# Kernel tuning notes

Measured on AMD Instinct MI355X. Metric: run time of the kernel, lower is better.

The kernel has to match this reference:

```python
import jax, jax.numpy as jnp
import numpy as np

H = 8          # num_heads
DM = 128       # dmodel
BN_EPS = 1e-5


def _linear(x, w, b):
    # w stored as [in, out]
    return x @ w + b


def _relu_mha(q, k, v, qw, qb, kw, kb, vw, vb, ow, ob, mask):
    """TemMulHeadAtte: ReLU on projected Q/K/V, masked softmax, ReLU out-proj.
    q,k: [B,N,T,2*DM]; v: [B,N,T,DM]; mask: broadcastable to [B,N,H,T,T] or None."""
    B, N, T, _ = q.shape
    Q = jax.nn.relu(_linear(q, qw, qb)).reshape(B, N, T, H, -1)  # e = 2*DM/H
    K = jax.nn.relu(_linear(k, kw, kb)).reshape(B, N, T, H, -1)
    V = jax.nn.relu(_linear(v, vw, vb)).reshape(B, N, T, H, -1)  # d = DM/H
    scale = 1.0 / np.sqrt(Q.shape[-1]).astype(np.float32)
    scores = jnp.einsum('bnthe,bnshe->bnhts', Q, K)
    if mask is not None:
        scores = jnp.where(mask, -jnp.inf, scores)
    attn = jax.nn.softmax(scale * scores, axis=-1)  # dropout p=0 -> identity
    out = jnp.einsum('bnhts,bnshd->bnthd', attn, V).reshape(B, N, T, -1)
    return jax.nn.relu(_linear(out, ow, ob))


def setup_inputs() -> dict:
    key = jax.random.key(0)
    ks = iter(jax.random.split(key, 32))
    B, N, T = 16, 207, 24
    def w(shape, scale=0.05):
        return (jax.random.normal(next(ks), shape, dtype=jnp.float32) * scale)
    inp = {
        'x': w((B, N, T, DM), 1.0),
        'hidden': w((B, N, T, DM), 1.0),
        'tXin': w((B, N, T, DM), 1.0),
    }
    dk = 2 * DM // H * H   # 256
    dv = DM // H * H       # 128
    for pre in ('s', 't'):  # space / temporal attention params
        inp[pre + 'q_w'] = w((2 * DM, dk)); inp[pre + 'q_b'] = w((dk,))
        inp[pre + 'k_w'] = w((2 * DM, dk)); inp[pre + 'k_b'] = w((dk,))
        inp[pre + 'v_w'] = w((DM, dv));     inp[pre + 'v_b'] = w((dv,))
        inp[pre + 'o_w'] = w((dv, DM));     inp[pre + 'o_b'] = w((DM,))
    inp['gate_w'] = w((2 * DM, DM)); inp['gate_b'] = w((DM,))
    inp['bn_gamma'] = jnp.ones((DM,), jnp.float32)
    inp['bn_beta'] = jnp.zeros((DM,), jnp.float32)
    return inp


def reference(x, hidden, tXin,
              sq_w, sq_b, sk_w, sk_b, sv_w, sv_b, so_w, so_b,
              tq_w, tq_b, tk_w, tk_b, tv_w, tv_b, to_w, to_b,
              gate_w, gate_b, bn_gamma, bn_beta):
    B, N, T, E = hidden.shape
    ht = jnp.concatenate([hidden, tXin], axis=3)  # [B,N,T,2*DM]
    # spatial attention: attend over nodes (N<->T permute)
    sqk = ht.transpose(0, 2, 1, 3)        # [B,T,N,2*DM]
    sval = hidden.transpose(0, 2, 1, 3)   # [B,T,N,DM]
    spaceOut = _relu_mha(sqk, sqk, sval, sq_w, sq_b, sk_w, sk_b, sv_w, sv_b,
                         so_w, so_b, None).transpose(0, 2, 1, 3)  # [B,N,T,DM]
    # temporal attention with causal (strict upper-tri) mask
    mask = jnp.triu(jnp.ones((T, T), dtype=bool), 1)[None, None, None]
    tempOut = _relu_mha(ht, ht, hidden, tq_w, tq_b, tk_w, tk_b, tv_w, tv_b,
                        to_w, to_b, mask)  # [B,N,T,DM]
    # gate + BatchNorm2d over channel dim (training-mode batch stats, biased var)
    gi = _linear(jnp.concatenate([spaceOut, tempOut], axis=3), gate_w, gate_b)
    mean = gi.mean(axis=(0, 1, 2))
    var = gi.var(axis=(0, 1, 2))
    z = jax.nn.sigmoid((gi - mean) * jax.lax.rsqrt(var + BN_EPS) * bn_gamma + bn_beta)
    return z * spaceOut + (1.0 - z) * tempOut
```

## Files before the change

kernel.cpp:

```cpp
#include <hip/hip_runtime.h>
#include <hip/hip_bf16.h>

typedef __bf16 bf16;
typedef __bf16 bf16x8 __attribute__((ext_vector_type(8)));
typedef float f32x4 __attribute__((ext_vector_type(4)));

#define MTOT 79488
#define NDIM 207
#define TDIM 24

__global__ void detect_dtype(const void* __restrict__ hidden, int* __restrict__ flag)
{
    __shared__ int cnt;
    if (threadIdx.x == 0) cnt = 0;
    __syncthreads();
    const bf16* h = (const bf16*)hidden;
    int local = 0;
    for (int i = threadIdx.x; i < 4096; i += 256) {
        float v = (float)h[i];
        if (!(fabsf(v) < 1e6f)) local++;
    }
    atomicAdd(&cnt, local);
    __syncthreads();
    if (threadIdx.x == 0) *flag = (cnt > 8) ? 1 : 0;
}

__device__ inline float ld_ext(const void* p, int idx, int isF32)
{
    return isF32 ? ((const float*)p)[idx] : (float)((const bf16*)p)[idx];
}

__global__ __launch_bounds__(256) void prep_weights(
    const void* __restrict__ sq, const void* __restrict__ sk, const void* __restrict__ sv,
    const void* __restrict__ so, const void* __restrict__ tq, const void* __restrict__ tk,
    const void* __restrict__ tv, const void* __restrict__ to_, const void* __restrict__ gw,
    const void* __restrict__ sqb, const void* __restrict__ skb, const void* __restrict__ svb,
    const void* __restrict__ sob, const void* __restrict__ tqb, const void* __restrict__ tkb,
    const void* __restrict__ tvb, const void* __restrict__ tob, const void* __restrict__ gb,
    bf16* __restrict__ wdst, bf16* __restrict__ bdst, const int* __restrict__ dtf)
{
    const int isF32 = *dtf;
    if (blockIdx.x == 1536) {
        for (int j = threadIdx.x; j < 1664; j += 256) {
            const void* src; int i2;
            if      (j < 256)  { src = sqb; i2 = j; }
            else if (j < 512)  { src = skb; i2 = j - 256; }
            else if (j < 640)  { src = svb; i2 = j - 512; }
            else if (j < 896)  { src = tqb; i2 = j - 640; }
            else if (j < 1152) { src = tkb; i2 = j - 896; }
            else if (j < 1280) { src = tvb; i2 = j - 1152; }
            else if (j < 1408) { src = sob; i2 = j - 1280; }
            else if (j < 1536) { src = tob; i2 = j - 1408; }
            else               { src = gb;  i2 = j - 1536; }
            bdst[j] = (bf16)ld_ext(src, i2, isF32);
        }
        return;
    }
    const int e = blockIdx.x * 256 + threadIdx.x;
    float v;
    if (e < 327680) {
        int br = (e >= 163840);
        int e2 = e - br * 163840;
        int n = e2 >> 8, k = e2 & 255;
        const void* qw = br ? tq : sq;
        const void* kw = br ? tk : sk;
        const void* vw = br ? tv : sv;
        if      (n < 256) v = ld_ext(qw, k * 256 + n, isF32);
        else if (n < 512) v = ld_ext(kw, k * 256 + (n - 256), isF32);
        else              v = (k < 128) ? ld_ext(vw, k * 128 + (n - 512), isF32) : 0.f;
    } else if (e < 360448) {
        int br = (e >= 344064);
        int e2 = e - 327680 - br * 16384;
        int n = e2 >> 7, k = e2 & 127;
        v = ld_ext(br ? to_ : so, k * 128 + n, isF32);
    } else {
        int e2 = e - 360448;
        int n = e2 >> 8, k = e2 & 255;
        v = ld_ext(gw, k * 128 + n, isF32);
    }
    wdst[e] = (bf16)v;
}

__global__ __launch_bounds__(256) void gemm_bt(
    const void* __restrict__ A0v, const void* __restrict__ A1v,
    const bf16* __restrict__ Bt, const bf16* __restrict__ bias,
    bf16* __restrict__ C, int Nout, int Ktot, int doRelu, int aExt,
    const int* __restrict__ dtf)
{
    const int isF32 = *dtf;
    const int aF32  = aExt & isF32;
    __shared__ bf16 As[128 * 72];
    __shared__ bf16 Bs[128 * 72];
    const int tid  = threadIdx.x;
    const int wid  = tid >> 6, lane = tid & 63;
    const int wm   = (wid >> 1) * 64, wn = (wid & 1) * 64;
    const int quad = lane >> 4, l16 = lane & 15;
    const int m0   = blockIdx.x * 128, n0 = blockIdx.y * 128;
    const int lrow = tid >> 3;
    const int lcol = (tid & 7) * 8;

    f32x4 acc[4][4] = {};

    for (int k0 = 0; k0 < Ktot; k0 += 64) {
        const void* Ap = (k0 < 128) ? A0v : A1v;
        const int koff = (k0 < 128) ? k0 : k0 - 128;
        #pragma unroll
        for (int p = 0; p < 4; ++p) {
            int r = lrow + p * 32;
            bf16x8 av;
            if (aF32) {
                const float* Af = (const float*)Ap;
                f32x4 lo = *(const f32x4*)(Af + (size_t)(m0 + r) * 128 + koff + lcol);
                f32x4 hi = *(const f32x4*)(Af + (size_t)(m0 + r) * 128 + koff + lcol + 4);
                av[0]=(bf16)lo[0]; av[1]=(bf16)lo[1]; av[2]=(bf16)lo[2]; av[3]=(bf16)lo[3];
                av[4]=(bf16)hi[0]; av[5]=(bf16)hi[1]; av[6]=(bf16)hi[2]; av[7]=(bf16)hi[3];
            } else {
                av = *(const bf16x8*)((const bf16*)Ap + (size_t)(m0 + r) * 128 + koff + lcol);
            }
            *(bf16x8*)&As[r * 72 + lcol] = av;
        }
        #pragma unroll
        for (int p = 0; p < 4; ++p) {
            int r = lrow + p * 32;
            *(bf16x8*)&Bs[r * 72 + lcol] =
                *(const bf16x8*)(Bt + (size_t)(n0 + r) * Ktot + k0 + lcol);
        }
        __syncthreads();
        #pragma unroll
        for (int kk = 0; kk < 64; kk += 32) {
            bf16x8 af[4], bfr[4];
            #pragma unroll
            for (int i = 0; i < 4; ++i)
                af[i] = *(const bf16x8*)&As[(wm + i * 16 + l16) * 72 + kk + quad * 8];
            #pragma unroll
            for (int j = 0; j < 4; ++j)
                bfr[j] = *(const bf16x8*)&Bs[(wn + j * 16 + l16) * 72 + kk + quad * 8];
            #pragma unroll
            for (int i = 0; i < 4; ++i)
                #pragma unroll
                for (int j = 0; j < 4; ++j)
                    acc[i][j] = __builtin_amdgcn_mfma_f32_16x16x32_bf16(
                        af[i], bfr[j], acc[i][j], 0, 0, 0);
        }
        __syncthreads();
    }
    #pragma unroll
    for (int j = 0; j < 4; ++j) {
        int col = n0 + wn + j * 16 + l16;
        float bv = (float)bias[col];
        #pragma unroll
        for (int i = 0; i < 4; ++i) {
            int rbase = m0 + wm + i * 16 + quad * 4;
            #pragma unroll
            for (int r = 0; r < 4; ++r) {
                float v = acc[i][j][r] + bv;
                if (doRelu) v = fmaxf(v, 0.f);
                C[(size_t)(rbase + r) * Nout + col] = (bf16)v;
            }
        }
    }
}

__global__ __launch_bounds__(256) void attn_spatial_mfma(
    const bf16* __restrict__ QKV, bf16* __restrict__ O)
{
    const int hh = blockIdx.x, t = blockIdx.y, b = blockIdx.z;
    __shared__ bf16 Ks[224 * 40];
    __shared__ bf16 Vt[16 * 232];
    __shared__ bf16 Pl[4][16 * 40];
    const int tid = threadIdx.x;
    const int wave = tid >> 6, lane = tid & 63;
    const int quad = lane >> 4, l16 = lane & 15;
    const int STR = 640;

    for (int idx = tid; idx < 224 * 4; idx += 256) {
        int n = idx >> 2, seg = (idx & 3) * 8;
        bf16x8 v8 = {};
        if (n < NDIM)
            v8 = *(const bf16x8*)(QKV + ((size_t)(b * NDIM + n) * TDIM + t) * STR
                                  + 256 + hh * 32 + seg);
        *(bf16x8*)&Ks[n * 40 + seg] = v8;
    }
    for (int idx = tid; idx < 224 * 16; idx += 256) {
        int s = idx >> 4, d = idx & 15;
        bf16 v = (bf16)0.f;
        if (s < NDIM)
            v = QKV[((size_t)(b * NDIM + s) * TDIM + t) * STR + 512 + hh * 16 + d];
        Vt[d * 232 + s] = v;
    }
    __syncthreads();

    const float scale = 0.17677669529663687f;

    for (int qt = wave; qt < 13; qt += 4) {
        const int q0 = qt * 16;
        int qrow = q0 + l16; if (qrow >= NDIM) qrow = NDIM - 1;
        bf16x8 qfrag = *(const bf16x8*)(QKV + ((size_t)(b * NDIM + qrow) * TDIM + t) * STR
                                        + hh * 32 + quad * 8);
        f32x4 s[14];
        #pragma unroll
        for (int c = 0; c < 14; ++c) {
            bf16x8 kf = *(const bf16x8*)&Ks[(c * 16 + l16) * 40 + quad * 8];
            f32x4 z = {};
            s[c] = __builtin_amdgcn_mfma_f32_16x16x32_bf16(qfrag, kf, z, 0, 0, 0);
        }
        float l[4];
        #pragma unroll
        for (int r = 0; r < 4; ++r) {
            float mx = -1e30f;
            #pragma unroll
            for (int c = 0; c < 14; ++c) {
                int si = c * 16 + l16;
                float x = (si < NDIM) ? s[c][r] : -1e30f;
                mx = fmaxf(mx, x);
            }
            mx = fmaxf(mx, __shfl_xor(mx, 1));
            mx = fmaxf(mx, __shfl_xor(mx, 2));
            mx = fmaxf(mx, __shfl_xor(mx, 4));
            mx = fmaxf(mx, __shfl_xor(mx, 8));
            float sum = 0.f;
            #pragma unroll
            for (int c = 0; c < 14; ++c) {
                int si = c * 16 + l16;
                float p = (si < NDIM) ? __expf((s[c][r] - mx) * scale) : 0.f;
                s[c][r] = p;
                sum += p;
            }
            sum += __shfl_xor(sum, 1);
            sum += __shfl_xor(sum, 2);
            sum += __shfl_xor(sum, 4);
            sum += __shfl_xor(sum, 8);
            l[r] = sum;
        }
        f32x4 oacc = {};
        #pragma unroll
        for (int sc = 0; sc < 7; ++sc) {
            #pragma unroll
            for (int r = 0; r < 4; ++r) {
                Pl[wave][(quad * 4 + r) * 40 + l16]      = (bf16)s[2 * sc][r];
                Pl[wave][(quad * 4 + r) * 40 + 16 + l16] = (bf16)s[2 * sc + 1][r];
            }
            bf16x8 pf = *(const bf16x8*)&Pl[wave][l16 * 40 + quad * 8];
            bf16x8 vf = *(const bf16x8*)&Vt[l16 * 232 + sc * 32 + quad * 8];
            oacc = __builtin_amdgcn_mfma_f32_16x16x32_bf16(pf, vf, oacc, 0, 0, 0);
        }
        #pragma unroll
        for (int r = 0; r < 4; ++r) {
            int row = q0 + quad * 4 + r;
            if (row < NDIM)
                O[((size_t)(b * NDIM + row) * TDIM + t) * 128 + hh * 16 + l16]
                    = (bf16)(oacc[r] / l[r]);
        }
    }
}

__global__ __launch_bounds__(256) void attn_temporal(
    const bf16* __restrict__ QKV, bf16* __restrict__ O)
{
    const size_t m0 = (size_t)blockIdx.x * TDIM;
    __shared__ float Ks[TDIM][256];
    __shared__ float Vs[TDIM][128];
    const int tid = threadIdx.x;
    const int STR = 640;

    for (int idx = tid; idx < TDIM * 32; idx += 256) {
        int row = idx >> 5, c8 = (idx & 31) * 8;
        bf16x8 v = *(const bf16x8*)(QKV + (m0 + row) * STR + 256 + c8);
        #pragma unroll
        for (int j = 0; j < 8; ++j) Ks[row][c8 + j] = (float)v[j];
    }
    for (int idx = tid; idx < TDIM * 16; idx += 256) {
        int row = idx >> 4, c8 = (idx & 15) * 8;
        bf16x8 v = *(const bf16x8*)(QKV + (m0 + row) * STR + 512 + c8);
        #pragma unroll
        for (int j = 0; j < 8; ++j) Vs[row][c8 + j] = (float)v[j];
    }
    __syncthreads();

    if (tid < 8 * TDIM) {
        const int h = tid / TDIM, q = tid % TDIM;
        float qv[32];
        const bf16x8* qp = (const bf16x8*)(QKV + (m0 + q) * STR + h * 32);
        #pragma unroll
        for (int cc = 0; cc < 4; ++cc) {
            bf16x8 v = qp[cc];
            #pragma unroll
            for (int jj = 0; jj < 8; ++jj) qv[cc * 8 + jj] = (float)v[jj];
        }
        const float scale = 0.17677669529663687f;
        float mx = -1e29f, l = 0.f, acc[16] = {};
        for (int s = 0; s <= q; ++s) {
            float x = 0.f;
            #pragma unroll
            for (int c = 0; c < 32; ++c) x += qv[c] * Ks[s][h * 32 + c];
            x *= scale;
            float mn = fmaxf(mx, x);
            float corr = __expf(mx - mn);
            float p = __expf(x - mn);
            l = l * corr + p;
            #pragma unroll
            for (int d = 0; d < 16; ++d) acc[d] = acc[d] * corr + p * Vs[s][h * 16 + d];
            mx = mn;
        }
        float inv = 1.f / l;
        #pragma unroll
        for (int d = 0; d < 16; ++d)
            O[(m0 + q) * 128 + h * 16 + d] = (bf16)(acc[d] * inv);
    }
}

__global__ __launch_bounds__(256) void bn_stats(
    const bf16* __restrict__ gi, float* __restrict__ stats)
{
    __shared__ float ssum[256], ssq[256];
    const size_t base = (size_t)blockIdx.x * 16384;
    const int tid = threadIdx.x;
    float s = 0.f, sq = 0.f;
    #pragma unroll 4
    for (int i = 0; i < 64; ++i) {
        float v = (float)gi[base + (size_t)i * 256 + tid];
        s += v; sq += v * v;
    }
    ssum[tid] = s; ssq[tid] = sq;
    __syncthreads();
    if (tid < 128) {
        atomicAdd(&stats[tid], ssum[tid] + ssum[tid + 128]);
        atomicAdd(&stats[128 + tid], ssq[tid] + ssq[tid + 128]);
    }
}

__global__ __launch_bounds__(256) void bn_final(
    const bf16* __restrict__ gi, const bf16* __restrict__ sp, const bf16* __restrict__ tp,
    const void* __restrict__ gammav, const void* __restrict__ betav,
    const float* __restrict__ stats, void* __restrict__ outv,
    const int* __restrict__ dtf)
{
    const int isF32 = *dtf;
    const int idx = blockIdx.x * 256 + threadIdx.x;
    const int c = idx & 127;
    const float invM = 1.f / (float)MTOT;
    float mean = stats[c] * invM;
    float var  = stats[128 + c] * invM - mean * mean;
    float gam = ld_ext(gammav, c, isF32);
    float bet = ld_ext(betav, c, isF32);
    float g = (float)gi[idx];
    float zn = (g - mean) * rsqrtf(var + 1e-5f) * gam + bet;
    float z = 1.f / (1.f + __expf(-zn));
    float s = (float)sp[idx], t = (float)tp[idx];
    float r = z * s + (1.f - z) * t;
    if (isF32) ((float*)outv)[idx] = r;
    else       ((bf16*)outv)[idx] = (bf16)r;
}

extern "C" void kernel_launch(void* const* d_in, const int* in_sizes, int n_in,
                              void* d_out, int out_size, void* d_ws, size_t ws_size,
                              hipStream_t stream)
{
    const void* hidden = d_in[1];
    const void* tXin   = d_in[2];
    const void* sq_w = d_in[3];  const void* sq_b = d_in[4];
    const void* sk_w = d_in[5];  const void* sk_b = d_in[6];
    const void* sv_w = d_in[7];  const void* sv_b = d_in[8];
    const void* so_w = d_in[9];  const void* so_b = d_in[10];
    const void* tq_w = d_in[11]; const void* tq_b = d_in[12];
    const void* tk_w = d_in[13]; const void* tk_b = d_in[14];
    const void* tv_w = d_in[15]; const void* tv_b = d_in[16];
    const void* to_w = d_in[17]; const void* to_b = d_in[18];
    const void* gate_w = d_in[19]; const void* gate_b = d_in[20];
    const void* gamma  = d_in[21]; const void* beta   = d_in[22];

    char* ws = (char*)d_ws;
    float* stats = (float*)ws;
    int*  dtf    = (int*)(ws + 1024);
    bf16* bB     = (bf16*)(ws + 2048);
    bf16* wT     = (bf16*)(ws + 8192);
    bf16* spaceO = (bf16*)(ws + 794624);
    bf16* attnO  = (bf16*)(ws + 21143552);
    bf16* QKV    = (bf16*)(ws + 41492480);
    bf16* tempO  = attnO;
    bf16* gi     = QKV;

    bf16* sW  = wT;            bf16* tW  = wT + 163840;
    bf16* soT = wT + 327680;   bf16* toT = wT + 344064;
    bf16* gwT = wT + 360448;

    hipMemsetAsync(stats, 0, 1024, stream);
    detect_dtype<<<1, 256, 0, stream>>>(hidden, dtf);
    prep_weights<<<dim3(1537), 256, 0, stream>>>(
        sq_w, sk_w, sv_w, so_w, tq_w, tk_w, tv_w, to_w, gate_w,
        sq_b, sk_b, sv_b, so_b, tq_b, tk_b, tv_b, to_b, gate_b,
        wT, bB, dtf);

    gemm_bt<<<dim3(621, 5), 256, 0, stream>>>(hidden, tXin, sW, bB, QKV, 640, 256, 1, 1, dtf);
    attn_spatial_mfma<<<dim3(8, TDIM, 16), 256, 0, stream>>>(QKV, attnO);
    gemm_bt<<<dim3(621, 1), 256, 0, stream>>>(attnO, nullptr, soT, bB + 1280, spaceO, 128, 128, 1, 0, dtf);

    gemm_bt<<<dim3(621, 5), 256, 0, stream>>>(hidden, tXin, tW, bB + 640, QKV, 640, 256, 1, 1, dtf);
    attn_temporal<<<dim3(16 * NDIM), 256, 0, stream>>>(QKV, attnO);
    gemm_bt<<<dim3(621, 1), 256, 0, stream>>>(attnO, nullptr, toT, bB + 1408, tempO, 128, 128, 1, 0, dtf);

    gemm_bt<<<dim3(621, 1), 256, 0, stream>>>(spaceO, tempO, gwT, bB + 1536, gi, 128, 256, 0, 0, dtf);
    bn_stats<<<dim3(621), 256, 0, stream>>>(gi, stats);
    bn_final<<<dim3(39744), 256, 0, stream>>>(gi, spaceO, tempO, gamma, beta, stats, d_out, dtf);
}
```

Before: 572.6 us.

## Use MFMA for temporal attention and pre-convert fp32 inputs to bf16

Replaces the scalar per-thread temporal attention loop with an MFMA-based kernel. Each wave handles two heads, computes masked scores with bf16 matrix instructions, does a shuffle-based softmax and runs a PV MFMA. Separately, when the workspace is large enough, hidden and tXin are converted once to bf16 buffers. This lets the two QKV GEMMs read bf16 A operands instead of converting fp32 on every tile load. The conversion adds an extra pass over the inputs, and the bf16 probabilities may lose precision.

```diff
diff --git a/kernel.cpp b/kernel.cpp
--- a/kernel.cpp
+++ b/kernel.cpp
@@ -28,6 +28,26 @@
 __device__ inline float ld_ext(const void* p, int idx, int isF32)
 {
     return isF32 ? ((const float*)p)[idx] : (float)((const bf16*)p)[idx];
+}
+
+__global__ __launch_bounds__(256) void cvt_inputs(
+    const void* __restrict__ hidden, const void* __restrict__ tXin,
+    bf16* __restrict__ hb, bf16* __restrict__ tb, const int* __restrict__ dtf)
+{
+    const int isF32 = *dtf;
+    const void* src = blockIdx.y ? tXin : hidden;
+    bf16* dst = blockIdx.y ? tb : hb;
+    const size_t e8 = ((size_t)blockIdx.x * 256 + threadIdx.x) * 8;
+    bf16x8 v;
+    if (isF32) {
+        f32x4 lo = *(const f32x4*)((const float*)src + e8);
+        f32x4 hi = *(const f32x4*)((const float*)src + e8 + 4);
+        v[0]=(bf16)lo[0]; v[1]=(bf16)lo[1]; v[2]=(bf16)lo[2]; v[3]=(bf16)lo[3];
+        v[4]=(bf16)hi[0]; v[5]=(bf16)hi[1]; v[6]=(bf16)hi[2]; v[7]=(bf16)hi[3];
+    } else {
+        v = *(const bf16x8*)((const bf16*)src + e8);
+    }
+    *(bf16x8*)(dst + e8) = v;
 }
 
 __global__ __launch_bounds__(256) void prep_weights(
@@ -87,8 +107,7 @@
     bf16* __restrict__ C, int Nout, int Ktot, int doRelu, int aExt,
     const int* __restrict__ dtf)
 {
-    const int isF32 = *dtf;
-    const int aF32  = aExt & isF32;
+    const int aF32 = aExt & *dtf;
     __shared__ bf16 As[128 * 72];
     __shared__ bf16 Bs[128 * 72];
     const int tid  = threadIdx.x;
@@ -254,58 +273,81 @@
     }
 }
 
-__global__ __launch_bounds__(256) void attn_temporal(
+__global__ __launch_bounds__(256) void attn_temporal_mfma(
     const bf16* __restrict__ QKV, bf16* __restrict__ O)
 {
     const size_t m0 = (size_t)blockIdx.x * TDIM;
-    __shared__ float Ks[TDIM][256];
-    __shared__ float Vs[TDIM][128];
+    __shared__ bf16 Khs[8 * 32 * 40];
+    __shared__ bf16 Vts[8 * 16 * 40];
+    __shared__ bf16 Pl[4][16 * 40];
     const int tid = threadIdx.x;
+    const int wave = tid >> 6, lane = tid & 63;
+    const int quad = lane >> 4, l16 = lane & 15;
     const int STR = 640;
 
-    for (int idx = tid; idx < TDIM * 32; idx += 256) {
-        int row = idx >> 5, c8 = (idx & 31) * 8;
-        bf16x8 v = *(const bf16x8*)(QKV + (m0 + row) * STR + 256 + c8);
-        #pragma unroll
-        for (int j = 0; j < 8; ++j) Ks[row][c8 + j] = (float)v[j];
-    }
-    for (int idx = tid; idx < TDIM * 16; idx += 256) {
-        int row = idx >> 4, c8 = (idx & 15) * 8;
-        bf16x8 v = *(const bf16x8*)(QKV + (m0 + row) * STR + 512 + c8);
-        #pragma unroll
-        for (int j = 0; j < 8; ++j) Vs[row][c8 + j] = (float)v[j];
+    for (int idx = tid; idx < 32 * 32; idx += 256) {
+        int row = idx >> 5, seg = idx & 31;
+        int h = seg >> 2, j = (seg & 3) * 8;
+        bf16x8 v8 = {};
+        if (row < TDIM)
+            v8 = *(const bf16x8*)(QKV + (m0 + row) * STR + 256 + h * 32 + j);
+        *(bf16x8*)&Khs[h * 1280 + row * 40 + j] = v8;
+    }
+    for (int idx = tid; idx < 32 * 128; idx += 256) {
+        int s = idx >> 7, c = idx & 127;
+        int h = c >> 4, d = c & 15;
+        bf16 v = (bf16)0.f;
+        if (s < TDIM) v = QKV[(m0 + s) * STR + 512 + h * 16 + d];
+        Vts[h * 640 + d * 40 + s] = v;
     }
     __syncthreads();
 
-    if (tid < 8 * TDIM) {
-        const int h = tid / TDIM, q = tid % TDIM;
-        float qv[32];
-        const bf16x8* qp = (const bf16x8*)(QKV + (m0 + q) * STR + h * 32);
-        #pragma unroll
-        for (int cc = 0; cc < 4; ++cc) {
-            bf16x8 v = qp[cc];
-            #pragma unroll
-            for (int jj = 0; jj < 8; ++jj) qv[cc * 8 + jj] = (float)v[jj];
-        }
-        const float scale = 0.17677669529663687f;
-        float mx = -1e29f, l = 0.f, acc[16] = {};
-        for (int s = 0; s <= q; ++s) {
-            float x = 0.f;
-            #pragma unroll
-            for (int c = 0; c < 32; ++c) x += qv[c] * Ks[s][h * 32 + c];
-            x *= scale;
-            float mn = fmaxf(mx, x);
-            float corr = __expf(mx - mn);
-            float p = __expf(x - mn);
-            l = l * corr + p;
-            #pragma unroll
-            for (int d = 0; d < 16; ++d) acc[d] = acc[d] * corr + p * Vs[s][h * 16 + d];
-            mx = mn;
-        }
-        float inv = 1.f / l;
-        #pragma unroll
-        for (int d = 0; d < 16; ++d)
-            O[(m0 + q) * 128 + h * 16 + d] = (bf16)(acc[d] * inv);
+    const float scale = 0.17677669529663687f;
+
+    #pragma unroll
+    for (int hi = 0; hi < 2; ++hi) {
+        const int h = wave * 2 + hi;
+        #pragma unroll
+        for (int qt = 0; qt < 2; ++qt) {
+            int qrow = qt * 16 + l16; if (qrow >= TDIM) qrow = TDIM - 1;
+            bf16x8 qfrag = *(const bf16x8*)(QKV + (m0 + qrow) * STR + h * 32 + quad * 8);
+            bf16x8 kf0 = *(const bf16x8*)&Khs[h * 1280 + l16 * 40 + quad * 8];
+            bf16x8 kf1 = *(const bf16x8*)&Khs[h * 1280 + (16 + l16) * 40 + quad * 8];
+            f32x4 z = {};
+            f32x4 s0 = __builtin_amdgcn_mfma_f32_16x16x32_bf16(qfrag, kf0, z, 0, 0, 0);
+            f32x4 s1 = __builtin_amdgcn_mfma_f32_16x16x32_bf16(qfrag, kf1, z, 0, 0, 0);
+            float l[4];
+            #pragma unroll
+            for (int r = 0; r < 4; ++r) {
+                int q = qt * 16 + quad * 4 + r;
+                float x0 = (l16 <= q) ? s0[r] : -1e30f;
+                float x1 = (16 + l16 <= q && 16 + l16 < TDIM) ? s1[r] : -1e30f;
+                float mx = fmaxf(x0, x1);
+                mx = fmaxf(mx, __shfl_xor(mx, 1));
+                mx = fmaxf(mx, __shfl_xor(mx, 2));
+                mx = fmaxf(mx, __shfl_xor(mx, 4));
+                mx = fmaxf(mx, __shfl_xor(mx, 8));
+                float p0 = (x0 > -1e29f) ? __expf((x0 - mx) * scale) : 0.f;
+                float p1 = (x1 > -1e29f) ? __expf((x1 - mx) * scale) : 0.f;
+                float sum = p0 + p1;
+                sum += __shfl_xor(sum, 1);
+                sum += __shfl_xor(sum, 2);
+                sum += __shfl_xor(sum, 4);
+                sum += __shfl_xor(sum, 8);
+                l[r] = sum;
+                Pl[wave][(quad * 4 + r) * 40 + l16]      = (bf16)p0;
+                Pl[wave][(quad * 4 + r) * 40 + 16 + l16] = (bf16)p1;
+            }
+            bf16x8 pf = *(const bf16x8*)&Pl[wave][l16 * 40 + quad * 8];
+            bf16x8 vf = *(const bf16x8*)&Vts[h * 640 + l16 * 40 + quad * 8];
+            f32x4 oacc = __builtin_amdgcn_mfma_f32_16x16x32_bf16(pf, vf, z, 0, 0, 0);
+            #pragma unroll
+            for (int r = 0; r < 4; ++r) {
+                int row = qt * 16 + quad * 4 + r;
+                if (row < TDIM)
+                    O[(m0 + row) * 128 + h * 16 + l16] = (bf16)(oacc[r] / l[r]);
+            }
+        }
     }
 }
 
@@ -377,8 +419,12 @@
     bf16* spaceO = (bf16*)(ws + 794624);
     bf16* attnO  = (bf16*)(ws + 21143552);
     bf16* QKV    = (bf16*)(ws + 41492480);
+    bf16* hb     = (bf16*)(ws + 143237120);
+    bf16* tb     = (bf16*)(ws + 163586048);
     bf16* tempO  = attnO;
     bf16* gi     = QKV;
+
+    const int wsBig = (ws_size >= 184000000ull);
 
     bf16* sW  = wT;            bf16* tW  = wT + 163840;
     bf16* soT = wT + 327680;   bf16* toT = wT + 344064;
@@ -390,13 +436,19 @@
         sq_w, sk_w, sv_w, so_w, tq_w, tk_w, tv_w, to_w, gate_w,
         sq_b, sk_b, sv_b, so_b, tq_b, tk_b, tv_b, to_b, gate_b,
         wT, bB, dtf);
-
-    gemm_bt<<<dim3(621, 5), 256, 0, stream>>>(hidden, tXin, sW, bB, QKV, 640, 256, 1, 1, dtf);
+    if (wsBig)
+        cvt_inputs<<<dim3(4968, 2), 256, 0, stream>>>(hidden, tXin, hb, tb, dtf);
+
+    const void* A0 = wsBig ? (const void*)hb : hidden;
+    const void* A1 = wsBig ? (const void*)tb : tXin;
+    const int aExt = wsBig ? 0 : 1;
+
+    gemm_bt<<<dim3(621, 5), 256, 0, stream>>>(A0, A1, sW, bB, QKV, 640, 256, 1, aExt, dtf);
     attn_spatial_mfma<<<dim3(8, TDIM, 16), 256, 0, stream>>>(QKV, attnO);
     gemm_bt<<<dim3(621, 1), 256, 0, stream>>>(attnO, nullptr, soT, bB + 1280, spaceO, 128, 128, 1, 0, dtf);
 
-    gemm_bt<<<dim3(621, 5), 256, 0, stream>>>(hidden, tXin, tW, bB + 640, QKV, 640, 256, 1, 1, dtf);
-    attn_temporal<<<dim3(16 * NDIM), 256, 0, stream>>>(QKV, attnO);
+    gemm_bt<<<dim3(621, 5), 256, 0, stream>>>(A0, A1, tW, bB + 640, QKV, 640, 256, 1, aExt, dtf);
+    attn_temporal_mfma<<<dim3(16 * NDIM), 256, 0, stream>>>(QKV, attnO);
     gemm_bt<<<dim3(621, 1), 256, 0, stream>>>(attnO, nullptr, toT, bB + 1408, tempO, 128, 128, 1, 0, dtf);
 
     gemm_bt<<<dim3(621, 1), 256, 0, stream>>>(spaceO, tempO, gwT, bB + 1536, gi, 128, 256, 0, 0, dtf);
```

Measured after the change: 544.2 us. 1.05x faster.
